# Performance work log

Measured on AMD Instinct MI355X. Metric: run time of the kernel, lower is better.

Reference implementation:

```python
import jax, jax.numpy as jnp
import numpy as np
import math

B, C, H, T, S = 2, 1024, 16, 2048, 2048
DH = C // H  # 64


def setup_inputs() -> dict:
    key = jax.random.key(0)
    ks = jax.random.split(key, 10)
    target = jax.random.normal(ks[0], (B, C, T), dtype=jnp.float32)
    source = jax.random.normal(ks[1], (B, C, S), dtype=jnp.float32)
    target_mask = (jax.random.uniform(ks[2], (B, 1, T)) < 0.9).astype(jnp.float32)
    source_mask = (jax.random.uniform(ks[3], (B, 1, S)) < 0.9).astype(jnp.float32)
    scale = 1.0 / math.sqrt(C)
    Wq = jax.random.normal(ks[4], (C, C), dtype=jnp.float32) * scale
    bq = jnp.zeros((C,), dtype=jnp.float32)
    Wk = jax.random.normal(ks[5], (C, C), dtype=jnp.float32) * scale
    bk = jnp.zeros((C,), dtype=jnp.float32)
    Wv = jax.random.normal(ks[6], (C, C), dtype=jnp.float32) * scale
    bv = jnp.zeros((C,), dtype=jnp.float32)
    return {"target": target, "source": source, "target_mask": target_mask,
            "source_mask": source_mask, "Wq": Wq, "bq": bq, "Wk": Wk, "bk": bk,
            "Wv": Wv, "bv": bv}


def _proj(W, b, x):
    # 1x1 Conv1d == pointwise channel mixing: [B,C,L] -> [B,C,L]
    return jnp.einsum('oc,bcl->bol', W, x) + b[None, :, None]


def reference(target, source, target_mask, source_mask, Wq, bq, Wk, bk, Wv, bv):
    q = _proj(Wq, bq, target).reshape(B, H, DH, T)
    k = _proj(Wk, bk, source).reshape(B, H, DH, S)
    v = _proj(Wv, bv, source).reshape(B, H, DH, S)
    # dot: [B,H,T,S], scaled by sqrt(d_head) (key.size(2) in torch)
    dot = jnp.einsum('bhdt,bhds->bhts', q, k) / math.sqrt(DH)
    # available mask [B,1,T,S], broadcast over heads
    avail = jnp.einsum('bjt,bjs->bjts', target_mask, source_mask)
    dot = avail * dot - (1.0 - avail) * 1.0e6
    # NOTE: original torch code overwrites the masked amap with a plain
    # softmax of the (masked) dot; we reproduce that exactly.
    amap = jax.nn.softmax(dot, axis=-1)
    out = jnp.einsum('bhts,bhds->bhdt', amap, v)  # [B,H,DH,T]
    return out.reshape(B, C, T)
```

## Files before the change

kernel.cpp:

```cpp
#include <hip/hip_runtime.h>

#define BB 2
#define CC 1024
#define HH 16
#define TT 2048
#define SS 2048
#define LL 2048
#define C2MASK 1442695.0f
#define NT_TILES (SS / 64)

typedef unsigned short u16;
typedef unsigned int u32;
typedef __attribute__((ext_vector_type(8))) short short8;
typedef __attribute__((ext_vector_type(4))) float f32x4;
typedef __attribute__((ext_vector_type(4))) unsigned short us4;
typedef __attribute__((ext_vector_type(2))) unsigned int u32x2;

__device__ __forceinline__ u16 f2bf(float f) {
    union { float f; unsigned int i; } x; x.f = f;
    unsigned int r = x.i + 0x7FFFu + ((x.i >> 16) & 1u);
    return (u16)(r >> 16);
}
__device__ __forceinline__ float exp2_hw(float x) {
    float r;
    asm("v_exp_f32 %0, %1" : "=v"(r) : "v"(x));
    return r;
}
__device__ __forceinline__ float max3f(float a, float b, float c) {
    float r;
    asm("v_max3_f32 %0, %1, %2, %3" : "=v"(r) : "v"(a), "v"(b), "v"(c));
    return r;
}
__device__ __forceinline__ u32 cvtpk_bf16(float lo, float hi) {
    u32 r;
    asm("v_cvt_pk_bf16_f32 %0, %1, %2" : "=v"(r) : "v"(lo), "v"(hi));
    return r;
}
__device__ __forceinline__ void gload_lds16(const u16* g, u16* l) {
    __builtin_amdgcn_global_load_lds(
        (const __attribute__((address_space(1))) unsigned int*)g,
        (__attribute__((address_space(3))) unsigned int*)l, 16, 0, 0);
}

__global__ __launch_bounds__(256) void qkv_gemm(
    const float* __restrict__ target, const float* __restrict__ source,
    const float* __restrict__ tmaskp, const float* __restrict__ smaskp,
    const float* __restrict__ Wq, const float* __restrict__ bq,
    const float* __restrict__ Wk, const float* __restrict__ bk,
    const float* __restrict__ Wv, const float* __restrict__ bv,
    u16* __restrict__ Qb, u16* __restrict__ Kb, u16* __restrict__ Vb,
    float* __restrict__ sbias, float* __restrict__ zrow)
{
    const int p = blockIdx.z >> 1;
    const int b = blockIdx.z & 1;

    if (blockIdx.x == 0 && blockIdx.y == 0 && p == 0) {
        const float* sm = smaskp + (size_t)b * SS;
        float* sb = sbias + (size_t)b * SS;
        for (int i = threadIdx.x; i < SS; i += 256) {
            sb[i] = (sm[i] > 0.5f) ? 0.0f : -C2MASK;
            if (b == 0) zrow[i] = 0.0f;
        }
    }

    const float* W    = (p == 0) ? Wq : (p == 1) ? Wk : Wv;
    const float* bias = (p == 0) ? bq : (p == 1) ? bk : bv;
    const float* X    = ((p == 0) ? target : source) + (size_t)b * CC * LL;

    const int m0 = blockIdx.y * 128;
    const int n0 = blockIdx.x * 128;

    __shared__ __align__(16) u16 As[128 * 72];
    __shared__ __align__(16) u16 Bs[128 * 72];

    const int tid  = threadIdx.x;
    const int lane = tid & 63;
    const int wid  = tid >> 6;
    const int ln   = lane & 15;
    const int q    = lane >> 4;
    const int wm   = (wid >> 1) * 64;
    const int wn   = (wid & 1) * 64;

    f32x4 acc[4][4];
#pragma unroll
    for (int i = 0; i < 4; i++)
#pragma unroll
        for (int j = 0; j < 4; j++) acc[i][j] = (f32x4){0.f, 0.f, 0.f, 0.f};

    const int arow_s = tid >> 3;
    const int ach    = tid & 7;
    const int lp     = tid & 31;
    const int cp0    = tid >> 5;

    for (int k0 = 0; k0 < CC; k0 += 64) {
        __syncthreads();
#pragma unroll
        for (int i = 0; i < 4; i++) {
            const int row = arow_s + i * 32;
            const float* wp = W + (size_t)(m0 + row) * CC + k0 + ach * 8;
            f32x4 w0 = *(const f32x4*)wp;
            f32x4 w1 = *(const f32x4*)(wp + 4);
            short8 av;
#pragma unroll
            for (int j = 0; j < 4; j++) { av[j] = (short)f2bf(w0[j]); av[4 + j] = (short)f2bf(w1[j]); }
            *(short8*)(As + row * 72 + ach * 8) = av;
        }
#pragma unroll
        for (int i = 0; i < 2; i++) {
            const int cpi = cp0 + i * 8;
            const float* xp = X + (size_t)(k0 + cpi * 4) * LL + n0 + lp * 4;
            f32x4 x0 = *(const f32x4*)(xp);
            f32x4 x1 = *(const f32x4*)(xp + LL);
            f32x4 x2 = *(const f32x4*)(xp + 2 * LL);
            f32x4 x3 = *(const f32x4*)(xp + 3 * LL);
#pragma unroll
            for (int u = 0; u < 4; u++) {
                us4 w;
                w[0] = f2bf(x0[u]); w[1] = f2bf(x1[u]);
                w[2] = f2bf(x2[u]); w[3] = f2bf(x3[u]);
                *(us4*)(Bs + (lp * 4 + u) * 72 + cpi * 4) = w;
            }
        }
        __syncthreads();

        short8 aF[4][2], bF[4][2];
#pragma unroll
        for (int mt = 0; mt < 4; mt++) {
            aF[mt][0] = *(const short8*)(As + (wm + mt*16 + ln) * 72 + q * 8);
            aF[mt][1] = *(const short8*)(As + (wm + mt*16 + ln) * 72 + 32 + q * 8);
        }
#pragma unroll
        for (int nt = 0; nt < 4; nt++) {
            bF[nt][0] = *(const short8*)(Bs + (wn + nt*16 + ln) * 72 + q * 8);
            bF[nt][1] = *(const short8*)(Bs + (wn + nt*16 + ln) * 72 + 32 + q * 8);
        }
#pragma unroll
        for (int mt = 0; mt < 4; mt++)
#pragma unroll
            for (int nt = 0; nt < 4; nt++) {
                acc[mt][nt] = __builtin_amdgcn_mfma_f32_16x16x32_bf16(aF[mt][0], bF[nt][0], acc[mt][nt], 0, 0, 0);
                acc[mt][nt] = __builtin_amdgcn_mfma_f32_16x16x32_bf16(aF[mt][1], bF[nt][1], acc[mt][nt], 0, 0, 0);
            }
    }

    const float oscale = (p == 0) ? 0.18033688011112042f : 1.0f;
#pragma unroll
    for (int mt = 0; mt < 4; mt++) {
        const int o_base = m0 + wm + mt * 16 + q * 4;
        float bsf[4];
#pragma unroll
        for (int r = 0; r < 4; r++) bsf[r] = bias[o_base + r];
#pragma unroll
        for (int nt = 0; nt < 4; nt++) {
            const int l = n0 + wn + nt * 16 + ln;
            if (p == 2) {
#pragma unroll
                for (int r = 0; r < 4; r++)
                    Vb[((size_t)b * CC + o_base + r) * SS + l] = f2bf(acc[mt][nt][r] + bsf[r]);
            } else {
                const int h = o_base >> 6;
                const int d = o_base & 63;
                u16* dst = (p == 0) ? Qb : Kb;
                float sc2 = oscale;
                if (p == 0) sc2 = oscale * tmaskp[(size_t)b * TT + l];
                us4 pk;
#pragma unroll
                for (int r = 0; r < 4; r++) pk[r] = (u16)f2bf((acc[mt][nt][r] + bsf[r]) * sc2);
                *(us4*)(dst + ((size_t)(b * HH + h) * TT + l) * 64 + d) = pk;
            }
        }
    }
}

__global__ __launch_bounds__(256, 4) void attn_k(
    const u16* __restrict__ Qb, const u16* __restrict__ Kb, const u16* __restrict__ Vb,
    const float* __restrict__ tmask, const float* __restrict__ sbias,
    const float* __restrict__ zrow, float* __restrict__ out)
{
    __shared__ __align__(16) u16 Ks[2][64 * 64];
    __shared__ __align__(16) u16 Vs[2][64 * 64];
    __shared__ __align__(16) u16 Ps[4][16 * 64];

    const int tid  = threadIdx.x;
    const int wid  = tid >> 6;
    const int lane = tid & 63;
    const int ln   = lane & 15;
    const int q    = lane >> 4;

    const int idx   = blockIdx.x;
    const int xcd   = idx & 7;
    const int rest  = idx >> 3;
    const int ttile = rest & 31;
    const int bh    = (rest >> 5) * 8 + xcd;
    const int b     = bh >> 4;
    const int h     = bh & 15;
    const int t0    = ttile * 64 + wid * 16;

    const u16* Qp = Qb + (size_t)bh * TT * 64;
    const u16* Kp = Kb + (size_t)bh * SS * 64;
    const u16* Vp = Vb + ((size_t)b * CC + h * 64) * SS;

    const float tm = tmask[(size_t)b * TT + t0 + ln];
    const float* bp = (tm > 0.5f) ? (sbias + (size_t)b * SS) : zrow;

    const int r0  = tid >> 3;
    const int c0  = tid & 7;
    const int cs0 = c0 ^ (r0 & 7);
    const u16* kg0 = Kp + (size_t)r0 * 64 + cs0 * 8;
    const u16* kg1 = Kp + (size_t)(r0 + 32) * 64 + cs0 * 8;
    const u16* vg0 = Vp + (size_t)r0 * SS + cs0 * 8;
    const u16* vg1 = Vp + (size_t)(r0 + 32) * SS + cs0 * 8;
    const int lw0 = wid * 512;
    const int lw1 = 2048 + wid * 512;

#define STAGE(buf, sn) do {                                         \
        gload_lds16(kg0 + (size_t)(sn) * 64, &Ks[buf][lw0]);        \
        gload_lds16(kg1 + (size_t)(sn) * 64, &Ks[buf][lw1]);        \
        gload_lds16(vg0 + (sn), &Vs[buf][lw0]);                     \
        gload_lds16(vg1 + (sn), &Vs[buf][lw1]);                     \
    } while (0)

    short8 qB0 = *(const short8*)(Qp + (size_t)(t0 + ln) * 64 + q * 8);
    short8 qB1 = *(const short8*)(Qp + (size_t)(t0 + ln) * 64 + 32 + q * 8);

    float mR = -3.0e38f, lR = 0.f;
    f32x4 oA[4];
#pragma unroll
    for (int dt = 0; dt < 4; dt++) oA[dt] = (f32x4){0.f, 0.f, 0.f, 0.f};

    const int sx0 = ((q ^ (ln & 7)) << 3);
    const int sx1 = (((q + 4) ^ (ln & 7)) << 3);

    u16* pw = Ps[wid];

    STAGE(0, 0);

    int cur = 0;
#pragma unroll 2
    for (int it = 0; it < NT_TILES; ++it) {
        const int s0 = it * 64;
        __syncthreads();
        if (it + 1 < NT_TILES) STAGE(cur ^ 1, s0 + 64);

        const u16* KsB = Ks[cur];
        const u16* VsB = Vs[cur];

        f32x4 sc[4];
#pragma unroll
        for (int nt = 0; nt < 4; nt++) {
            const u16* kr = KsB + (nt * 16 + ln) * 64;
            short8 k0 = *(const short8*)(kr + sx0);
            short8 k1 = *(const short8*)(kr + sx1);
            f32x4 bias = *(const f32x4*)(bp + s0 + nt * 16 + q * 4);
            sc[nt] = __builtin_amdgcn_mfma_f32_16x16x32_bf16(k0, qB0, bias, 0, 0, 0);
            sc[nt] = __builtin_amdgcn_mfma_f32_16x16x32_bf16(k1, qB1, sc[nt], 0, 0, 0);
        }

        float m4[4];
#pragma unroll
        for (int nt = 0; nt < 4; nt++)
            m4[nt] = fmaxf(max3f(sc[nt][0], sc[nt][1], sc[nt][2]), sc[nt][3]);
        float m_ = fmaxf(max3f(m4[0], m4[1], m4[2]), m4[3]);
        m_ = fmaxf(m_, __shfl_xor(m_, 16, 64));
        m_ = fmaxf(m_, __shfl_xor(m_, 32, 64));

        if (!__all(m_ - mR <= 8.0f)) {
            const float mN = fmaxf(mR, m_);
            const float al = exp2_hw(mR - mN);
            lR *= al;
#pragma unroll
            for (int dt = 0; dt < 4; dt++) oA[dt] *= al;
            mR = mN;
        }

        float s4[4];
#pragma unroll
        for (int nt = 0; nt < 4; nt++) {
#pragma unroll
            for (int r = 0; r < 4; r++) sc[nt][r] = exp2_hw(sc[nt][r] - mR);
            s4[nt] = (sc[nt][0] + sc[nt][1]) + (sc[nt][2] + sc[nt][3]);
        }
        float s_ = (s4[0] + s4[1]) + (s4[2] + s4[3]);
        s_ += __shfl_xor(s_, 16, 64);
        s_ += __shfl_xor(s_, 32, 64);
        lR += s_;

#pragma unroll
        for (int nt = 0; nt < 4; nt++) {
            u32x2 w;
            w[0] = cvtpk_bf16(sc[nt][0], sc[nt][1]);
            w[1] = cvtpk_bf16(sc[nt][2], sc[nt][3]);
            const int chunk = (nt << 1) | (q >> 1);
            *(u32x2*)(pw + ln * 64 + ((chunk ^ (ln & 7)) << 3) + ((q & 1) << 2)) = w;
        }
        short8 pB0 = *(const short8*)(pw + ln * 64 + sx0);
        short8 pB1 = *(const short8*)(pw + ln * 64 + sx1);
#pragma unroll
        for (int dt = 0; dt < 4; dt++) {
            const u16* vr = VsB + (dt * 16 + ln) * 64;
            short8 v0 = *(const short8*)(vr + sx0);
            short8 v1 = *(const short8*)(vr + sx1);
            oA[dt] = __builtin_amdgcn_mfma_f32_16x16x32_bf16(v0, pB0, oA[dt], 0, 0, 0);
            oA[dt] = __builtin_amdgcn_mfma_f32_16x16x32_bf16(v1, pB1, oA[dt], 0, 0, 0);
        }
        cur ^= 1;
    }
#undef STAGE

    const float inv = 1.0f / lR;
#pragma unroll
    for (int dt = 0; dt < 4; dt++)
#pragma unroll
        for (int r = 0; r < 4; r++)
            out[((size_t)b * CC + h * 64 + dt * 16 + q * 4 + r) * TT + t0 + ln] =
                oA[dt][r] * inv;
}

extern "C" void kernel_launch(void* const* d_in, const int* in_sizes, int n_in,
                              void* d_out, int out_size, void* d_ws, size_t ws_size,
                              hipStream_t stream)
{
    const float* target = (const float*)d_in[0];
    const float* source = (const float*)d_in[1];
    const float* tmask  = (const float*)d_in[2];
    const float* smask  = (const float*)d_in[3];
    const float* Wq = (const float*)d_in[4];
    const float* bq = (const float*)d_in[5];
    const float* Wk = (const float*)d_in[6];
    const float* bk = (const float*)d_in[7];
    const float* Wv = (const float*)d_in[8];
    const float* bv = (const float*)d_in[9];

    u16* ws = (u16*)d_ws;
    const size_t N1 = (size_t)BB * CC * TT;
    u16* Qb = ws;
    u16* Kb = ws + N1;
    u16* Vb = ws + 2 * N1;
    float* sbias = (float*)(ws + 3 * N1);
    float* zrow  = sbias + 2 * SS;

    qkv_gemm<<<dim3(TT/128, CC/128, 6), dim3(256, 1, 1), 0, stream>>>(
        target, source, tmask, smask, Wq, bq, Wk, bk, Wv, bv, Qb, Kb, Vb, sbias, zrow);
    attn_k<<<dim3(BB*HH*(TT/64), 1, 1), dim3(256, 1, 1), 0, stream>>>(
        Qb, Kb, Vb, tmask, sbias, zrow, (float*)d_out);
}
```

Before: 232.4 us.

## Pre-convert inputs and weights to bf16 and stream GEMM tiles via global_load_lds

Adds a prep kernel that converts Wq/Wk/Wv to bf16 and transposes target/source into bf16 [L,C] layout. The QKV GEMM then loads tiles directly into LDS with global_load_lds using an XOR-swizzled layout, instead of loading fp32, converting in registers and storing to padded LDS. This removes the conversion work and the strided transposing stores from the GEMM inner loop and halves the bytes the GEMM reads per tile. In exchange it adds an extra kernel launch and a full extra read and write pass over the inputs.

```diff
diff --git a/kernel.cpp b/kernel.cpp
--- a/kernel.cpp
+++ b/kernel.cpp
@@ -15,6 +15,7 @@
 typedef __attribute__((ext_vector_type(4))) float f32x4;
 typedef __attribute__((ext_vector_type(4))) unsigned short us4;
 typedef __attribute__((ext_vector_type(2))) unsigned int u32x2;
+typedef __attribute__((ext_vector_type(4))) unsigned int u32x4;
 
 __device__ __forceinline__ u16 f2bf(float f) {
     union { float f; unsigned int i; } x; x.f = f;
@@ -42,36 +43,95 @@
         (__attribute__((address_space(3))) unsigned int*)l, 16, 0, 0);
 }
 
-__global__ __launch_bounds__(256) void qkv_gemm(
+__global__ __launch_bounds__(256) void prep(
     const float* __restrict__ target, const float* __restrict__ source,
-    const float* __restrict__ tmaskp, const float* __restrict__ smaskp,
-    const float* __restrict__ Wq, const float* __restrict__ bq,
-    const float* __restrict__ Wk, const float* __restrict__ bk,
-    const float* __restrict__ Wv, const float* __restrict__ bv,
-    u16* __restrict__ Qb, u16* __restrict__ Kb, u16* __restrict__ Vb,
+    const float* __restrict__ smaskp,
+    const float* __restrict__ Wq, const float* __restrict__ Wk, const float* __restrict__ Wv,
+    u16* __restrict__ Wb, u16* __restrict__ Tt, u16* __restrict__ St,
     float* __restrict__ sbias, float* __restrict__ zrow)
 {
+    __shared__ float xs[64][65];
+    const int tid = threadIdx.x;
+    const int bid = blockIdx.x;
+
+    if (bid < 2048) {
+        const int img  = bid >> 9;
+        const int tile = bid & 511;
+        const int ct = tile >> 5, lt = tile & 31;
+        const int c0 = ct * 64, l0 = lt * 64;
+        const float* src = ((img < 2) ? target : source) + (size_t)(img & 1) * CC * LL;
+        u16* dst = ((img < 2) ? Tt : St) + (size_t)(img & 1) * LL * CC;
+
+        const int i = tid >> 2, seg = (tid & 3) * 16;
+        const float* g = src + (size_t)(c0 + i) * LL + l0 + seg;
+        f32x4 a0 = *(const f32x4*)g;
+        f32x4 a1 = *(const f32x4*)(g + 4);
+        f32x4 a2 = *(const f32x4*)(g + 8);
+        f32x4 a3 = *(const f32x4*)(g + 12);
+#pragma unroll
+        for (int j = 0; j < 4; j++) {
+            xs[i][seg + j]      = a0[j];
+            xs[i][seg + 4 + j]  = a1[j];
+            xs[i][seg + 8 + j]  = a2[j];
+            xs[i][seg + 12 + j] = a3[j];
+        }
+        __syncthreads();
+
+        const int l = tid >> 2, cseg = (tid & 3) * 16;
+        float f[16];
+#pragma unroll
+        for (int j = 0; j < 16; j++) f[j] = xs[cseg + j][l];
+        u32x4 o0, o1;
+#pragma unroll
+        for (int k = 0; k < 4; k++) {
+            o0[k] = cvtpk_bf16(f[2 * k], f[2 * k + 1]);
+            o1[k] = cvtpk_bf16(f[8 + 2 * k], f[9 + 2 * k]);
+        }
+        u16* d = dst + (size_t)(l0 + l) * CC + c0 + cseg;
+        *(u32x4*)d = o0;
+        *(u32x4*)(d + 8) = o1;
+    } else {
+        const int wblk = bid - 2048;
+        const size_t idx = (size_t)wblk * 2048 + tid * 8;
+        const int m = (int)(idx >> 20);
+        const size_t rem = idx & 1048575;
+        const float* srcp = ((m == 0) ? Wq : (m == 1) ? Wk : Wv) + rem;
+        f32x4 a = *(const f32x4*)srcp;
+        f32x4 c = *(const f32x4*)(srcp + 4);
+        u32x4 o;
+        o[0] = cvtpk_bf16(a[0], a[1]); o[1] = cvtpk_bf16(a[2], a[3]);
+        o[2] = cvtpk_bf16(c[0], c[1]); o[3] = cvtpk_bf16(c[2], c[3]);
+        *(u32x4*)(Wb + ((size_t)m << 20) + rem) = o;
+
+        if (wblk < 2) {
+            const int b = wblk;
+            const float* sm = smaskp + (size_t)b * SS;
+            float* sb = sbias + (size_t)b * SS;
+            for (int s = tid; s < SS; s += 256) {
+                sb[s] = (sm[s] > 0.5f) ? 0.0f : -C2MASK;
+                if (b == 0) zrow[s] = 0.0f;
+            }
+        }
+    }
+}
+
+__global__ __launch_bounds__(256) void qkv_gemm(
+    const u16* __restrict__ Wb, const u16* __restrict__ Tt, const u16* __restrict__ St,
+    const float* __restrict__ bq, const float* __restrict__ bk, const float* __restrict__ bv,
+    const float* __restrict__ tmaskp,
+    u16* __restrict__ Qb, u16* __restrict__ Kb, u16* __restrict__ Vb)
+{
+    __shared__ __align__(16) u16 As[128 * 64];
+    __shared__ __align__(16) u16 Bs[128 * 64];
+
     const int p = blockIdx.z >> 1;
     const int b = blockIdx.z & 1;
-
-    if (blockIdx.x == 0 && blockIdx.y == 0 && p == 0) {
-        const float* sm = smaskp + (size_t)b * SS;
-        float* sb = sbias + (size_t)b * SS;
-        for (int i = threadIdx.x; i < SS; i += 256) {
-            sb[i] = (sm[i] > 0.5f) ? 0.0f : -C2MASK;
-            if (b == 0) zrow[i] = 0.0f;
-        }
-    }
-
-    const float* W    = (p == 0) ? Wq : (p == 1) ? Wk : Wv;
-    const float* bias = (p == 0) ? bq : (p == 1) ? bk : bv;
-    const float* X    = ((p == 0) ? target : source) + (size_t)b * CC * LL;
-
     const int m0 = blockIdx.y * 128;
     const int n0 = blockIdx.x * 128;
 
-    __shared__ __align__(16) u16 As[128 * 72];
-    __shared__ __align__(16) u16 Bs[128 * 72];
+    const u16* A  = Wb + ((size_t)p << 20) + (size_t)m0 * CC;
+    const u16* Bx = ((p == 0) ? Tt : St) + (size_t)b * LL * CC + (size_t)n0 * CC;
+    const float* bias = (p == 0) ? bq : (p == 1) ? bk : bv;
 
     const int tid  = threadIdx.x;
     const int lane = tid & 63;
@@ -81,58 +141,42 @@
     const int wm   = (wid >> 1) * 64;
     const int wn   = (wid & 1) * 64;
 
+    const int r0 = tid >> 3;
+    const int cs = (tid & 7) ^ (r0 & 7);
+    const u16* ag = A  + (size_t)r0 * CC + cs * 8;
+    const u16* bg = Bx + (size_t)r0 * CC + cs * 8;
+    const int lb = wid * 512;
+
     f32x4 acc[4][4];
 #pragma unroll
     for (int i = 0; i < 4; i++)
 #pragma unroll
         for (int j = 0; j < 4; j++) acc[i][j] = (f32x4){0.f, 0.f, 0.f, 0.f};
 
-    const int arow_s = tid >> 3;
-    const int ach    = tid & 7;
-    const int lp     = tid & 31;
-    const int cp0    = tid >> 5;
+    const int sx0 = ((q ^ (ln & 7)) << 3);
+    const int sx1 = (((q + 4) ^ (ln & 7)) << 3);
 
     for (int k0 = 0; k0 < CC; k0 += 64) {
         __syncthreads();
 #pragma unroll
         for (int i = 0; i < 4; i++) {
-            const int row = arow_s + i * 32;
-            const float* wp = W + (size_t)(m0 + row) * CC + k0 + ach * 8;
-            f32x4 w0 = *(const f32x4*)wp;
-            f32x4 w1 = *(const f32x4*)(wp + 4);
-            short8 av;
-#pragma unroll
-            for (int j = 0; j < 4; j++) { av[j] = (short)f2bf(w0[j]); av[4 + j] = (short)f2bf(w1[j]); }
-            *(short8*)(As + row * 72 + ach * 8) = av;
-        }
-#pragma unroll
-        for (int i = 0; i < 2; i++) {
-            const int cpi = cp0 + i * 8;
-            const float* xp = X + (size_t)(k0 + cpi * 4) * LL + n0 + lp * 4;
-            f32x4 x0 = *(const f32x4*)(xp);
-            f32x4 x1 = *(const f32x4*)(xp + LL);
-            f32x4 x2 = *(const f32x4*)(xp + 2 * LL);
-            f32x4 x3 = *(const f32x4*)(xp + 3 * LL);
-#pragma unroll
-            for (int u = 0; u < 4; u++) {
-                us4 w;
-                w[0] = f2bf(x0[u]); w[1] = f2bf(x1[u]);
-                w[2] = f2bf(x2[u]); w[3] = f2bf(x3[u]);
-                *(us4*)(Bs + (lp * 4 + u) * 72 + cpi * 4) = w;
-            }
+            gload_lds16(ag + (size_t)i * 32 * CC + k0, &As[lb + i * 2048]);
+            gload_lds16(bg + (size_t)i * 32 * CC + k0, &Bs[lb + i * 2048]);
         }
         __syncthreads();
 
         short8 aF[4][2], bF[4][2];
 #pragma unroll
         for (int mt = 0; mt < 4; mt++) {
-            aF[mt][0] = *(const short8*)(As + (wm + mt*16 + ln) * 72 + q * 8);
-            aF[mt][1] = *(const short8*)(As + (wm + mt*16 + ln) * 72 + 32 + q * 8);
-        }
-#pragma unroll
-        for (int nt = 0; nt < 4; nt++) {
-            bF[nt][0] = *(const short8*)(Bs + (wn + nt*16 + ln) * 72 + q * 8);
-            bF[nt][1] = *(const short8*)(Bs + (wn + nt*16 + ln) * 72 + 32 + q * 8);
+            const u16* ar = As + (wm + mt * 16 + ln) * 64;
+            aF[mt][0] = *(const short8*)(ar + sx0);
+            aF[mt][1] = *(const short8*)(ar + sx1);
+        }
+#pragma unroll
+        for (int nt = 0; nt < 4; nt++) {
+            const u16* br = Bs + (wn + nt * 16 + ln) * 64;
+            bF[nt][0] = *(const short8*)(br + sx0);
+            bF[nt][1] = *(const short8*)(br + sx1);
         }
 #pragma unroll
         for (int mt = 0; mt < 4; mt++)
@@ -338,9 +382,14 @@
     u16* Vb = ws + 2 * N1;
     float* sbias = (float*)(ws + 3 * N1);
     float* zrow  = sbias + 2 * SS;
-
+    u16* Wb = (u16*)(zrow + SS);
+    u16* Tt = Wb + 3u * 1048576u;
+    u16* St = Tt + (size_t)BB * LL * CC;
+
+    prep<<<dim3(3584, 1, 1), dim3(256, 1, 1), 0, stream>>>(
+        target, source, smask, Wq, Wk, Wv, Wb, Tt, St, sbias, zrow);
     qkv_gemm<<<dim3(TT/128, CC/128, 6), dim3(256, 1, 1), 0, stream>>>(
-        target, source, tmask, smask, Wq, bq, Wk, bk, Wv, bv, Qb, Kb, Vb, sbias, zrow);
+        Wb, Tt, St, bq, bk, bv, tmask, Qb, Kb, Vb);
     attn_k<<<dim3(BB*HH*(TT/64), 1, 1), dim3(256, 1, 1), 0, stream>>>(
         Qb, Kb, Vb, tmask, sbias, zrow, (float*)d_out);
 }
```

Measured after the change: 205.3 us. -11.6%, faster.
